# Kernel optimization log

Measured on AMD Instinct MI355X. Metric: run time of the kernel, lower is better.

## Reference

```python
import jax, jax.numpy as jnp
import numpy as np

B, S, D_IN, D_OUT = 4, 4096, 1024, 64

def setup_inputs() -> dict:
    key = jax.random.key(0)
    ks = jax.random.split(key, 7)
    return {
        "x":  jax.random.normal(ks[0], (B, S, D_IN), dtype=jnp.float32),
        "Wq": jax.random.normal(ks[1], (D_IN, D_OUT), dtype=jnp.float32) * 0.02,
        "bq": jax.random.normal(ks[2], (D_OUT,), dtype=jnp.float32) * 0.02,
        "Wk": jax.random.normal(ks[3], (D_IN, D_OUT), dtype=jnp.float32) * 0.02,
        "bk": jax.random.normal(ks[4], (D_OUT,), dtype=jnp.float32) * 0.02,
        "Wv": jax.random.normal(ks[5], (D_IN, D_OUT), dtype=jnp.float32) * 0.02,
        "bv": jax.random.normal(ks[6], (D_OUT,), dtype=jnp.float32) * 0.02,
    }

def reference(x, Wq, bq, Wk, bk, Wv, bv):
    # x: [B, S, d_in]
    seq = x.shape[1]
    q = x @ Wq + bq            # [B, S, d_out]
    k = x @ Wk + bk
    v = x @ Wv + bv
    scores = jnp.einsum("bqd,bkd->bqk", q, k)          # [B, S, S]
    causal = jnp.triu(jnp.ones((seq, seq), dtype=bool), k=1)
    scores = jnp.where(causal[None, :, :], -jnp.inf, scores)
    # NOTE: original code scales by sqrt(token_len), not sqrt(d_out) (d_k = keys.shape[1])
    scale = jnp.sqrt(jnp.asarray(seq, dtype=scores.dtype))
    attn = jax.nn.softmax(scores / scale, axis=-1)      # [B, S, S]
    # dropout in the original is applied but its result is discarded -> no-op
    return jnp.einsum("bqk,bkd->bqd", attn, v)          # [B, S, d_out]
```

## Files before the change

### kernel.cpp

```cpp
#include <hip/hip_runtime.h>
#include <math.h>

#define B 4
#define S 4096
#define DIN 1024
#define DOUT 64
#define BS (B * S)

typedef __bf16 bf16;
typedef __bf16 bf16x4 __attribute__((ext_vector_type(4)));
typedef __bf16 bf16x8 __attribute__((ext_vector_type(8)));
typedef float f32x4 __attribute__((ext_vector_type(4)));

#define QSCALE 0.022542110013890053f

#define QS_OFF 0
#define KF_OFF (2u * 1024 * 1024)
#define VF_OFF (4u * 1024 * 1024)
#define WP_OFF (6u * 1024 * 1024)
#define OP_OFF (7u * 1024 * 1024)
#define LP_OFF (23u * 1024 * 1024)

__global__ __launch_bounds__(256) void wpack_kernel(
    const float* __restrict__ Wq, const float* __restrict__ Wk,
    const float* __restrict__ Wv, bf16* __restrict__ wp) {
  const int t = blockIdx.x * 256 + threadIdx.x;
  const int m = t >> 16;
  const int r = t & 65535;
  const int k = r >> 6;
  const int n64 = r & 63;
  const float* W = (m == 0) ? Wq : (m == 1) ? Wk : Wv;
  const float v = W[r];
  const int n = m * 64 + n64;
  const int nt = n >> 4;
  const int lane = ((k >> 3) & 3) * 16 + (n & 15);
  const int idx = ((nt * 32 + (k >> 5)) * 64 + lane) * 8 + (k & 7);
  wp[idx] = (bf16)v;
}

__global__ __launch_bounds__(256) void qkv_mfma_kernel(
    const float* __restrict__ x, const float* __restrict__ bq,
    const float* __restrict__ bk, const float* __restrict__ bv,
    const bf16* __restrict__ wp, bf16* __restrict__ Qs,
    bf16* __restrict__ KF, bf16* __restrict__ VF) {
  __shared__ __align__(16) bf16 xt[64][520];

  const int tid = threadIdx.x;
  const int wid = tid >> 6;
  const int lane = tid & 63;
  const int l15 = lane & 15;
  const int quad = lane >> 4;
  const int blk = blockIdx.x;

  const bf16x8* wp8 = (const bf16x8*)wp;

  f32x4 acc[3][4];
#pragma unroll
  for (int j = 0; j < 3; ++j)
#pragma unroll
    for (int s = 0; s < 4; ++s) acc[j][s] = (f32x4)(0.f);

  for (int ph = 0; ph < 2; ++ph) {
    if (ph) __syncthreads();
#pragma unroll
    for (int bst = 0; bst < 4; ++bst) {
      float4 v[8];
#pragma unroll
      for (int i = 0; i < 8; ++i) {
        const int ch = (bst * 8 + i) * 256 + tid;
        v[i] = *(const float4*)(x + (size_t)(blk * 64 + (ch >> 7)) * DIN +
                                ph * 512 + (ch & 127) * 4);
      }
#pragma unroll
      for (int i = 0; i < 8; ++i) {
        const int ch = (bst * 8 + i) * 256 + tid;
        bf16x4 c4;
        c4[0] = (bf16)v[i].x; c4[1] = (bf16)v[i].y;
        c4[2] = (bf16)v[i].z; c4[3] = (bf16)v[i].w;
        *(bf16x4*)&xt[ch >> 7][(ch & 127) * 4] = c4;
      }
    }
    __syncthreads();

#pragma unroll 4
    for (int kc = 0; kc < 16; ++kc) {
      bf16x8 bfr[3];
#pragma unroll
      for (int j = 0; j < 3; ++j)
        bfr[j] = wp8[((wid * 3 + j) * 32 + ph * 16 + kc) * 64 + lane];
      bf16x8 a[4];
#pragma unroll
      for (int s = 0; s < 4; ++s)
        a[s] = *(const bf16x8*)&xt[s * 16 + l15][quad * 8 + kc * 32];
#pragma unroll
      for (int j = 0; j < 3; ++j)
#pragma unroll
        for (int s = 0; s < 4; ++s)
          acc[j][s] = __builtin_amdgcn_mfma_f32_16x16x32_bf16(
              a[s], bfr[j], acc[j][s], 0, 0, 0);
    }
  }

#pragma unroll
  for (int j = 0; j < 3; ++j) {
    const int nt = wid * 3 + j;
    const int sel = nt >> 2;
    const int c = (nt & 3) * 16 + l15;
    const float bias = ((sel == 0) ? bq : (sel == 1) ? bk : bv)[c];
#pragma unroll
    for (int s = 0; s < 4; ++s) {
      const int row0 = blk * 64 + s * 16 + quad * 4;
      if (sel == 0) {
#pragma unroll
        for (int r = 0; r < 4; ++r)
          Qs[(size_t)(row0 + r) * DOUT + c] =
              (bf16)((acc[j][s][r] + bias) * QSCALE);
      } else if (sel == 1) {
        const size_t kb =
            ((size_t)(((row0 >> 6) * 4 + ((row0 >> 4) & 3)) * 2 + (c >> 5)) * 64 +
             ((c >> 3) & 3) * 16 + quad * 4) * 8 + (c & 7);
#pragma unroll
        for (int r = 0; r < 4; ++r)
          KF[kb + r * 8] = (bf16)(acc[j][s][r] + bias);
      } else {
        const size_t vb =
            ((size_t)(((row0 >> 6) * 2 + ((row0 >> 5) & 1)) * 4 + (c >> 4)) * 64 +
             (c & 15) + 16 * ((row0 >> 3) & 3)) * 8 + (row0 & 7);
        bf16x4 vv;
#pragma unroll
        for (int r = 0; r < 4; ++r) vv[r] = (bf16)(acc[j][s][r] + bias);
        *(bf16x4*)(VF + vb) = vv;
      }
    }
  }
}

__global__ __launch_bounds__(256) void attn_mfma_kernel(
    const bf16* __restrict__ Qs, const bf16* __restrict__ KFp,
    const bf16* __restrict__ VFp, bf16* __restrict__ Oh,
    float* __restrict__ lh) {
  __shared__ __align__(16) bf16 pw[4][32][72];

  const int tid = threadIdx.x;
  const int wid = tid >> 6;
  const int lane = tid & 63;
  const int l15 = lane & 15;
  const int quad = lane >> 4;
  const int b = blockIdx.x & 3;
  const int half = (blockIdx.x >> 2) & 1;
  const int s32 = 127 - (blockIdx.x >> 3);
  const int ntiles = (s32 >> 1) + 1;
  const int e = half * 4 + wid;
  const int t0 = (e * ntiles) >> 3;
  const int t1 = ((e + 1) * ntiles) >> 3;

  const bf16x8* KF8 = (const bf16x8*)KFp;
  const bf16x8* VF8 = (const bf16x8*)VFp;
  const int tb0 = b * 64;

  const bf16* Qb = Qs + ((size_t)b * S + s32 * 32) * DOUT;
  bf16x8 qf[2][2];
#pragma unroll
  for (int st = 0; st < 2; ++st)
#pragma unroll
    for (int k = 0; k < 2; ++k)
      qf[st][k] =
          *(const bf16x8*)(Qb + (st * 16 + l15) * DOUT + k * 32 + quad * 8);

  f32x4 o[2][4];
#pragma unroll
  for (int st = 0; st < 2; ++st)
#pragma unroll
    for (int i = 0; i < 4; ++i) o[st][i] = (f32x4)(0.f);
  f32x4 lsum[2] = {(f32x4)(0.f), (f32x4)(0.f)};

  for (int t = t0; t < t1; ++t) {
    const int tb = tb0 + t;
    bf16x8 kf[8], vf[8];
#pragma unroll
    for (int nt = 0; nt < 4; ++nt)
#pragma unroll
      for (int c = 0; c < 2; ++c)
        kf[nt * 2 + c] = KF8[(size_t)((tb * 4 + nt) * 2 + c) * 64 + lane];
#pragma unroll
    for (int c = 0; c < 2; ++c)
#pragma unroll
      for (int ntd = 0; ntd < 4; ++ntd)
        vf[c * 4 + ntd] = VF8[(size_t)((tb * 2 + c) * 4 + ntd) * 64 + lane];

    f32x4 s[2][4];
#pragma unroll
    for (int st = 0; st < 2; ++st)
#pragma unroll
      for (int nt = 0; nt < 4; ++nt) {
        s[st][nt] = __builtin_amdgcn_mfma_f32_16x16x32_bf16(
            qf[st][0], kf[nt * 2 + 0], (f32x4)(0.f), 0, 0, 0);
        s[st][nt] = __builtin_amdgcn_mfma_f32_16x16x32_bf16(
            qf[st][1], kf[nt * 2 + 1], s[st][nt], 0, 0, 0);
      }

    if (t == ntiles - 1) {
#pragma unroll
      for (int st = 0; st < 2; ++st)
#pragma unroll
        for (int nt = 0; nt < 4; ++nt) {
          const int key = t * 64 + nt * 16 + l15;
#pragma unroll
          for (int r = 0; r < 4; ++r) {
            const int qrow = s32 * 32 + st * 16 + quad * 4 + r;
            const float p = (key <= qrow) ? exp2f(fminf(s[st][nt][r], 44.f)) : 0.f;
            lsum[st][r] += p;
            pw[wid][st * 16 + quad * 4 + r][nt * 16 + l15] = (bf16)p;
          }
        }
    } else {
#pragma unroll
      for (int st = 0; st < 2; ++st)
#pragma unroll
        for (int nt = 0; nt < 4; ++nt)
#pragma unroll
          for (int r = 0; r < 4; ++r) {
            const float p = exp2f(fminf(s[st][nt][r], 44.f));
            lsum[st][r] += p;
            pw[wid][st * 16 + quad * 4 + r][nt * 16 + l15] = (bf16)p;
          }
    }

#pragma unroll
    for (int st = 0; st < 2; ++st) {
      const bf16x8 pf0 = *(const bf16x8*)&pw[wid][st * 16 + l15][quad * 8];
      const bf16x8 pf1 = *(const bf16x8*)&pw[wid][st * 16 + l15][32 + quad * 8];
#pragma unroll
      for (int ntd = 0; ntd < 4; ++ntd) {
        o[st][ntd] = __builtin_amdgcn_mfma_f32_16x16x32_bf16(
            pf0, vf[0 * 4 + ntd], o[st][ntd], 0, 0, 0);
        o[st][ntd] = __builtin_amdgcn_mfma_f32_16x16x32_bf16(
            pf1, vf[1 * 4 + ntd], o[st][ntd], 0, 0, 0);
      }
    }
  }

#pragma unroll
  for (int m = 1; m < 16; m <<= 1)
#pragma unroll
    for (int st = 0; st < 2; ++st)
#pragma unroll
      for (int r = 0; r < 4; ++r) lsum[st][r] += __shfl_xor(lsum[st][r], m, 64);

  const int slot = (b * 128 + s32) * 8 + e;
  if (l15 == 0) {
#pragma unroll
    for (int st = 0; st < 2; ++st)
#pragma unroll
      for (int r = 0; r < 4; ++r)
        lh[slot * 32 + st * 16 + quad * 4 + r] = lsum[st][r];
  }
#pragma unroll
  for (int st = 0; st < 2; ++st)
#pragma unroll
    for (int ntd = 0; ntd < 4; ++ntd)
#pragma unroll
      for (int r = 0; r < 4; ++r)
        Oh[(size_t)slot * 2048 + (st * 16 + quad * 4 + r) * 64 + ntd * 16 + l15] =
            (bf16)o[st][ntd][r];
}

__global__ __launch_bounds__(256) void combine_kernel(
    const bf16* __restrict__ Oh, const float* __restrict__ lh,
    float* __restrict__ out) {
  const int gid = blockIdx.x * 256 + threadIdx.x;
  const int token = gid >> 4;
  const int d4 = (gid & 15) * 4;
  const int b = token >> 12;
  const int s = token & 4095;
  const int s32 = s >> 5;
  const int qq = s & 31;
  const int slot0 = (b * 128 + s32) * 8;
  f32x4 acc = (f32x4)(0.f);
  float l = 0.f;
#pragma unroll
  for (int q = 0; q < 8; ++q) {
    const bf16x4 ov =
        *(const bf16x4*)(Oh + (size_t)(slot0 + q) * 2048 + qq * 64 + d4);
#pragma unroll
    for (int i = 0; i < 4; ++i) acc[i] += (float)ov[i];
    l += lh[(slot0 + q) * 32 + qq];
  }
  ((f32x4*)out)[gid] = acc * (1.f / l);
}

extern "C" void kernel_launch(void* const* d_in, const int* in_sizes, int n_in,
                              void* d_out, int out_size, void* d_ws,
                              size_t ws_size, hipStream_t stream) {
  const float* x  = (const float*)d_in[0];
  const float* Wq = (const float*)d_in[1];
  const float* bq = (const float*)d_in[2];
  const float* bk = (const float*)d_in[4];
  const float* Wk = (const float*)d_in[3];
  const float* Wv = (const float*)d_in[5];
  const float* bv = (const float*)d_in[6];
  float* out = (float*)d_out;

  char* ws = (char*)d_ws;
  bf16* Qs = (bf16*)(ws + QS_OFF);
  bf16* KF = (bf16*)(ws + KF_OFF);
  bf16* VF = (bf16*)(ws + VF_OFF);
  bf16* wp = (bf16*)(ws + WP_OFF);
  bf16* Oh = (bf16*)(ws + OP_OFF);
  float* lh = (float*)(ws + LP_OFF);

  wpack_kernel<<<768, 256, 0, stream>>>(Wq, Wk, Wv, wp);
  qkv_mfma_kernel<<<256, 256, 0, stream>>>(x, bq, bk, bv, wp, Qs, KF, VF);
  attn_mfma_kernel<<<1024, 256, 0, stream>>>(Qs, KF, VF, Oh, lh);
  combine_kernel<<<1024, 256, 0, stream>>>(Oh, lh, out);
}
```

Measured before the change: 147.4 us.

## Pre-cast x to bf16 and stream tiles into LDS via global_load_lds

Adds a separate kernel that converts x from fp32 to bf16 into workspace. The QKV projection then loads bf16 rows straight into shared memory using direct global-to-LDS loads, removing the per-thread register staging and conversion. This is meant to reduce load latency and instruction overhead in the QKV kernel. In exchange it adds an extra kernel launch and an extra round trip of x through memory.

```diff
diff --git a/kernel.cpp b/kernel.cpp
--- a/kernel.cpp
+++ b/kernel.cpp
@@ -11,6 +11,9 @@
 typedef __bf16 bf16x4 __attribute__((ext_vector_type(4)));
 typedef __bf16 bf16x8 __attribute__((ext_vector_type(8)));
 typedef float f32x4 __attribute__((ext_vector_type(4)));
+
+typedef __attribute__((address_space(1))) const unsigned int as1_u32;
+typedef __attribute__((address_space(3))) unsigned int as3_u32;
 
 #define QSCALE 0.022542110013890053f
 
@@ -20,6 +23,22 @@
 #define WP_OFF (6u * 1024 * 1024)
 #define OP_OFF (7u * 1024 * 1024)
 #define LP_OFF (23u * 1024 * 1024)
+#define XB_OFF (32u * 1024 * 1024)
+
+__global__ __launch_bounds__(256) void xcast_kernel(
+    const float* __restrict__ x, bf16* __restrict__ xb) {
+  const int t0 = blockIdx.x * 256 + threadIdx.x;
+#pragma unroll
+  for (int it = 0; it < 4; ++it) {
+    const size_t i = ((size_t)it * 524288 + t0) * 8;
+    const float4 a = *(const float4*)(x + i);
+    const float4 b = *(const float4*)(x + i + 4);
+    bf16x8 o;
+    o[0] = (bf16)a.x; o[1] = (bf16)a.y; o[2] = (bf16)a.z; o[3] = (bf16)a.w;
+    o[4] = (bf16)b.x; o[5] = (bf16)b.y; o[6] = (bf16)b.z; o[7] = (bf16)b.w;
+    *(bf16x8*)(xb + i) = o;
+  }
+}
 
 __global__ __launch_bounds__(256) void wpack_kernel(
     const float* __restrict__ Wq, const float* __restrict__ Wk,
@@ -39,7 +58,7 @@
 }
 
 __global__ __launch_bounds__(256) void qkv_mfma_kernel(
-    const float* __restrict__ x, const float* __restrict__ bq,
+    const bf16* __restrict__ xb, const float* __restrict__ bq,
     const float* __restrict__ bk, const float* __restrict__ bv,
     const bf16* __restrict__ wp, bf16* __restrict__ Qs,
     bf16* __restrict__ KF, bf16* __restrict__ VF) {
@@ -63,22 +82,12 @@
   for (int ph = 0; ph < 2; ++ph) {
     if (ph) __syncthreads();
 #pragma unroll
-    for (int bst = 0; bst < 4; ++bst) {
-      float4 v[8];
-#pragma unroll
-      for (int i = 0; i < 8; ++i) {
-        const int ch = (bst * 8 + i) * 256 + tid;
-        v[i] = *(const float4*)(x + (size_t)(blk * 64 + (ch >> 7)) * DIN +
-                                ph * 512 + (ch & 127) * 4);
-      }
-#pragma unroll
-      for (int i = 0; i < 8; ++i) {
-        const int ch = (bst * 8 + i) * 256 + tid;
-        bf16x4 c4;
-        c4[0] = (bf16)v[i].x; c4[1] = (bf16)v[i].y;
-        c4[2] = (bf16)v[i].z; c4[3] = (bf16)v[i].w;
-        *(bf16x4*)&xt[ch >> 7][(ch & 127) * 4] = c4;
-      }
+    for (int rr = 0; rr < 16; ++rr) {
+      const int row = rr * 4 + wid;
+      const bf16* gp =
+          xb + (size_t)(blk * 64 + row) * DIN + ph * 512 + lane * 8;
+      __builtin_amdgcn_global_load_lds((as1_u32*)gp, (as3_u32*)&xt[row][0],
+                                       16, 0, 0);
     }
     __syncthreads();
 
@@ -295,8 +304,8 @@
   const float* x  = (const float*)d_in[0];
   const float* Wq = (const float*)d_in[1];
   const float* bq = (const float*)d_in[2];
+  const float* Wk = (const float*)d_in[3];
   const float* bk = (const float*)d_in[4];
-  const float* Wk = (const float*)d_in[3];
   const float* Wv = (const float*)d_in[5];
   const float* bv = (const float*)d_in[6];
   float* out = (float*)d_out;
@@ -308,9 +317,11 @@
   bf16* wp = (bf16*)(ws + WP_OFF);
   bf16* Oh = (bf16*)(ws + OP_OFF);
   float* lh = (float*)(ws + LP_OFF);
-
+  bf16* xb = (bf16*)(ws + XB_OFF);
+
+  xcast_kernel<<<2048, 256, 0, stream>>>(x, xb);
   wpack_kernel<<<768, 256, 0, stream>>>(Wq, Wk, Wv, wp);
-  qkv_mfma_kernel<<<256, 256, 0, stream>>>(x, bq, bk, bv, wp, Qs, KF, VF);
+  qkv_mfma_kernel<<<256, 256, 0, stream>>>(xb, bq, bk, bv, wp, Qs, KF, VF);
   attn_mfma_kernel<<<1024, 256, 0, stream>>>(Qs, KF, VF, Oh, lh);
   combine_kernel<<<1024, 256, 0, stream>>>(Oh, lh, out);
 }
```

Result: slower. 160.5 us (+8.9%).
